# Performance work log

Hardware: AMD Instinct MI355X
Metric: run time of the kernel (lower is better)

The kernel has to match this reference:

```python
import jax, jax.numpy as jnp
import numpy as np

DIM = 768
NUM_HEADS = 12
DIM_HEAD = 64
INNER = NUM_HEADS * DIM_HEAD  # 768
SCALE = DIM_HEAD ** -0.5


def setup_inputs() -> dict:
    key = jax.random.key(0)
    k1, k2, k3 = jax.random.split(key, 3)
    B, N = 8, 1024
    x = jax.random.normal(k1, (B, N, DIM), dtype=jnp.float32)
    # Linear(dim, 3*inner_dim, bias=False): weight shape (out, in) torch-style
    w_qkv = jax.random.normal(k2, (3 * INNER, DIM), dtype=jnp.float32) * (DIM ** -0.5)
    # proj: Linear(inner_dim, dim, bias=False)
    w_proj = jax.random.normal(k3, (DIM, INNER), dtype=jnp.float32) * (INNER ** -0.5)
    return {"x": x, "w_qkv": w_qkv, "w_proj": w_proj}


def reference(x, w_qkv, w_proj):
    B, N, C = x.shape
    H, dh = NUM_HEADS, DIM_HEAD
    # qkv projection: (B,N,C) @ (C, 3*inner) -> (B,N,3*inner)
    qkv = jnp.einsum('bnc,oc->bno', x, w_qkv)
    qkv = qkv.reshape(B, N, 3, H, dh).transpose(2, 0, 3, 1, 4)  # (3,B,H,N,dh)
    q, k, v = qkv[0], qkv[1], qkv[2]
    # attention scores (B,H,N,N)
    attn_scores = jnp.einsum('bhnd,bhmd->bhnm', q, k) * SCALE
    attn_probs = jax.nn.softmax(attn_scores, axis=-1)
    # attention output (B,H,N,dh) -> (B,N,inner)
    attn_out = jnp.einsum('bhnm,bhmd->bhnd', attn_probs, v)
    attn_out = attn_out.transpose(0, 2, 1, 3).reshape(B, N, H * dh)
    out = jnp.einsum('bni,oi->bno', attn_out, w_proj)
    return out
```

## Files before the change

kernel.cpp:

```cpp
#include <hip/hip_runtime.h>
#include <stdint.h>

typedef unsigned short u16;
typedef __attribute__((ext_vector_type(8))) short short8;
typedef __attribute__((ext_vector_type(4))) short short4v;
typedef __attribute__((ext_vector_type(4))) float f32x4;

#define LOG2E 1.44269504088896340736f

#define Bb 8
#define NSEQ 1024
#define DIMC 768
#define NH 12
#define DH 64
#define INNER 768
#define MTOT (Bb*NSEQ)
#define QKVN (3*INNER)
#define HEADS_TOT (Bb*NH)
#define QKV_PART ((size_t)Bb*NH*NSEQ*DH)

static __device__ inline u16 f2bf(float f) {
    uint32_t u = __builtin_bit_cast(uint32_t, f);
    uint32_t r = (u + 0x7fffu + ((u >> 16) & 1u)) >> 16;
    return (u16)r;
}

static __device__ __forceinline__ uint32_t pkbf(float f0, float f1) {
    uint32_t u0 = __builtin_bit_cast(uint32_t, f0) + 0x8000u;
    uint32_t u1 = __builtin_bit_cast(uint32_t, f1) + 0x8000u;
    return __builtin_amdgcn_perm(u1, u0, 0x07060302u);
}

#if __has_builtin(__builtin_amdgcn_mfma_f32_16x16x16bf16_1k)
static __device__ __forceinline__ f32x4 mfma16(short4v a, short4v b, f32x4 c) {
    return __builtin_amdgcn_mfma_f32_16x16x16bf16_1k(a, b, c, 0, 0, 0);
}
#else
static __device__ __forceinline__ f32x4 mfma16(short4v a, short4v b, f32x4 c) {
    asm volatile("v_mfma_f32_16x16x16_bf16 %0, %1, %2, %0\n\ts_nop 7\n\ts_nop 7"
                 : "+v"(c) : "v"(a), "v"(b));
    return c;
}
#endif

typedef __attribute__((address_space(1))) const void gas_void;
typedef __attribute__((address_space(3))) void las_void;
static __device__ __forceinline__ void async16(u16* lds, const u16* g) {
    __builtin_amdgcn_global_load_lds((gas_void*)(uintptr_t)g,
                                     (las_void*)(uintptr_t)lds, 16, 0, 0);
}

template <int N>
static __device__ __forceinline__ void wait_vm() {
    __builtin_amdgcn_s_waitcnt(0x0f70 | N);
}

#define NX8  786432
#define NWQ8 221184
#define NWP8 73728
#define NCVT (NX8 + NWQ8 + NWP8)
__global__ __launch_bounds__(256) void cvt_all(const float* __restrict__ x,
                                               const float* __restrict__ wq,
                                               const float* __restrict__ wp,
                                               u16* __restrict__ xb,
                                               u16* __restrict__ wqb,
                                               u16* __restrict__ wpb) {
    int i = blockIdx.x * 256 + threadIdx.x;
    const float* s; u16* d; int j;
    if (i < NX8) { s = x; d = xb; j = i; }
    else if (i < NX8 + NWQ8) { s = wq; d = wqb; j = i - NX8; }
    else { s = wp; d = wpb; j = i - NX8 - NWQ8; }
    const float4* s4 = (const float4*)s;
    float4 a = s4[2 * j], b = s4[2 * j + 1];
    float v[8] = {a.x, a.y, a.z, a.w, b.x, b.y, b.z, b.w};
    u16 o[8];
#pragma unroll
    for (int t = 0; t < 8; t++) o[t] = f2bf(v[t]);
    ((uint4*)d)[j] = *(const uint4*)o;
}

#define BK 32
__global__ __launch_bounds__(512, 4) void gemm_qkv(const u16* __restrict__ A,
                                                   const u16* __restrict__ Bm,
                                                   u16* __restrict__ qkv) {
    __shared__ u16 As[3][128 * BK];
    __shared__ u16 Bs[3][256 * BK];
    const int tid = threadIdx.x;
    const int w = tid >> 6, lane = tid & 63, quad = lane >> 4, l16 = lane & 15;
    const int wr = w >> 2, wc = w & 3;
    const int bid = blockIdx.x + 9 * blockIdx.y;
    const int xcd = bid & 7, j9 = bid >> 3;
    const int m0 = (8 * xcd + j9 / 9) * 128;
    const int n0 = (j9 % 9) * 256;
    const int K = DIMC;

    const int rl = lane >> 2, cc = lane & 3;
    const int ra = w * 16 + rl;
    const u16* agp = A + (size_t)(m0 + ra) * K + ((cc - ((ra >> 1) & 3)) & 3) * 8;
    const int aslot = (w * 16) * BK;
    const u16* bgp[2]; int bslot[2];
#pragma unroll
    for (int j = 0; j < 2; j++) {
        int rb = w * 32 + j * 16 + rl;
        bgp[j] = Bm + (size_t)(n0 + rb) * K + ((cc - ((rb >> 1) & 3)) & 3) * 8;
        bslot[j] = (w * 32 + j * 16) * BK;
    }

    const int swz = ((quad + ((l16 >> 1) & 3)) & 3) * 8;
    int aoff[4], boff[4];
#pragma unroll
    for (int t = 0; t < 4; t++) {
        aoff[t] = (wr * 64 + t * 16 + l16) * BK + swz;
        boff[t] = (wc * 64 + t * 16 + l16) * BK + swz;
    }

#pragma unroll
    for (int tt = 0; tt < 2; tt++) {
        int kt = tt * BK;
        async16(&As[tt][aslot], agp + kt);
        async16(&Bs[tt][bslot[0]], bgp[0] + kt);
        async16(&Bs[tt][bslot[1]], bgp[1] + kt);
    }

    f32x4 acc[4][4] = {};
    const int NIT = K / BK;
    int cur = 0;
    for (int it = 0; it < NIT; ++it) {
        if (it < NIT - 1) wait_vm<3>();
        else              wait_vm<0>();
        __builtin_amdgcn_s_barrier();
        if (it < NIT - 2) {
            int pre = cur + 2; if (pre >= 3) pre -= 3;
            int ktn = (it + 2) * BK;
            async16(&As[pre][aslot], agp + ktn);
            async16(&Bs[pre][bslot[0]], bgp[0] + ktn);
            async16(&Bs[pre][bslot[1]], bgp[1] + ktn);
        }
        short8 af[4], bf[4];
#pragma unroll
        for (int t = 0; t < 4; t++) af[t] = *(const short8*)(&As[cur][aoff[t]]);
#pragma unroll
        for (int t = 0; t < 4; t++) bf[t] = *(const short8*)(&Bs[cur][boff[t]]);
#pragma unroll
        for (int mt = 0; mt < 4; mt++)
#pragma unroll
            for (int nt = 0; nt < 4; nt++)
                acc[mt][nt] = __builtin_amdgcn_mfma_f32_16x16x32_bf16(af[mt], bf[nt],
                                                                      acc[mt][nt], 0, 0, 0);
        cur = (cur == 2) ? 0 : cur + 1;
    }

#pragma unroll
    for (int nt = 0; nt < 4; nt++) {
        int o = n0 + wc * 64 + nt * 16 + l16;
        int which = o / 768;
        int rem = o - which * 768;
        int h = rem >> 6, d = rem & 63;
        if (which == 2) {
            u16* vt = qkv + 2 * QKV_PART;
#pragma unroll
            for (int mt = 0; mt < 4; mt++) {
                int m = m0 + wr * 64 + mt * 16 + quad * 4;
                int bb = m >> 10, ns = m & 1023;
                alignas(8) u16 pk[4];
#pragma unroll
                for (int r = 0; r < 4; r++) pk[r] = f2bf(acc[mt][nt][r]);
                *(uint2*)(vt + ((size_t)(bb * NH + h) * DH + d) * NSEQ + ns) =
                    *(const uint2*)pk;
            }
        } else {
            float sc = (which == 0) ? (0.125f * LOG2E) : 1.0f;
#pragma unroll
            for (int mt = 0; mt < 4; mt++)
#pragma unroll
                for (int r = 0; r < 4; r++) {
                    int m = m0 + wr * 64 + mt * 16 + quad * 4 + r;
                    int bb = m >> 10, ns = m & 1023;
                    size_t idx = (size_t)which * QKV_PART +
                                 (((size_t)(bb * NH + h) * NSEQ + ns) << 6) + d;
                    qkv[idx] = f2bf(acc[mt][nt][r] * sc);
                }
        }
    }
}

#define PBM 64
#define PBN 128
__global__ __launch_bounds__(256) void gemm_proj(const u16* __restrict__ A,
                                                 const u16* __restrict__ Bm,
                                                 float* __restrict__ Co) {
    __shared__ u16 As[3][PBM * BK];
    __shared__ u16 Bs[3][PBN * BK];
    const int tid = threadIdx.x;
    const int w = tid >> 6, lane = tid & 63, quad = lane >> 4, l16 = lane & 15;
    const int wr = w >> 1, wc = w & 1;
    const int m0 = blockIdx.y * PBM;
    const int n0 = blockIdx.x * PBN;
    const int K = INNER, N = DIMC;

    const int rl = lane >> 2, cc = lane & 3;
    const int ra = w * 16 + rl;
    const u16* agp = A + (size_t)(m0 + ra) * K + ((cc - ((ra >> 1) & 3)) & 3) * 8;
    const int aslot = (w * 16) * BK;
    const u16* bgp[2]; int bslot[2];
#pragma unroll
    for (int j = 0; j < 2; j++) {
        int rb = j * 64 + w * 16 + rl;
        bgp[j] = Bm + (size_t)(n0 + rb) * K + ((cc - ((rb >> 1) & 3)) & 3) * 8;
        bslot[j] = (j * 64 + w * 16) * BK;
    }
    const int swz = ((quad + ((l16 >> 1) & 3)) & 3) * 8;
    int aoff[2], boff[4];
#pragma unroll
    for (int t = 0; t < 2; t++) aoff[t] = (wr * 32 + t * 16 + l16) * BK + swz;
#pragma unroll
    for (int t = 0; t < 4; t++) boff[t] = (wc * 64 + t * 16 + l16) * BK + swz;

#pragma unroll
    for (int tt = 0; tt < 2; tt++) {
        int kt = tt * BK;
        async16(&As[tt][aslot], agp + kt);
        async16(&Bs[tt][bslot[0]], bgp[0] + kt);
        async16(&Bs[tt][bslot[1]], bgp[1] + kt);
    }

    f32x4 acc[2][4] = {};
    const int NIT = K / BK;
    int cur = 0;
    for (int it = 0; it < NIT; ++it) {
        if (it < NIT - 1) wait_vm<3>(); else wait_vm<0>();
        __builtin_amdgcn_s_barrier();
        if (it < NIT - 2) {
            int pre = cur + 2; if (pre >= 3) pre -= 3;
            int ktn = (it + 2) * BK;
            async16(&As[pre][aslot], agp + ktn);
            async16(&Bs[pre][bslot[0]], bgp[0] + ktn);
            async16(&Bs[pre][bslot[1]], bgp[1] + ktn);
        }
        short8 af[2], bf[4];
#pragma unroll
        for (int t = 0; t < 2; t++) af[t] = *(const short8*)(&As[cur][aoff[t]]);
#pragma unroll
        for (int t = 0; t < 4; t++) bf[t] = *(const short8*)(&Bs[cur][boff[t]]);
#pragma unroll
        for (int mt = 0; mt < 2; mt++)
#pragma unroll
            for (int nt = 0; nt < 4; nt++)
                acc[mt][nt] = __builtin_amdgcn_mfma_f32_16x16x32_bf16(af[mt], bf[nt],
                                                                      acc[mt][nt], 0, 0, 0);
        cur = (cur == 2) ? 0 : cur + 1;
    }
#pragma unroll
    for (int mt = 0; mt < 2; mt++)
#pragma unroll
        for (int nt = 0; nt < 4; nt++) {
            int o = n0 + wc * 64 + nt * 16 + l16;
#pragma unroll
            for (int r = 0; r < 4; r++) {
                int m = m0 + wr * 32 + mt * 16 + quad * 4 + r;
                Co[(size_t)m * N + o] = acc[mt][nt][r];
            }
        }
}

__global__ __launch_bounds__(256) void attn_kernel(const u16* __restrict__ qkv,
                                                   u16* __restrict__ attn) {
    __shared__ u16 Ks[3][64 * 64];
    __shared__ u16 Vs[3][64 * 64];

    const int tid = threadIdx.x;
    const int w = tid >> 6, lane = tid & 63, quad = lane >> 4, l16 = lane & 15;
    const int bh = blockIdx.x, qt = blockIdx.y;
    const size_t headoff = (size_t)bh * NSEQ * DH;
    const u16* Qp = qkv + headoff;
    const u16* Kp = qkv + QKV_PART + headoff;
    const u16* Vtp = qkv + 2 * QKV_PART + headoff;
    const int q0 = qt * 128 + w * 32;

    const int rl8 = lane >> 3, cc8 = lane & 7;
    const u16* kg[2]; const u16* vg[2]; int ksl[2];
#pragma unroll
    for (int j = 0; j < 2; j++) {
        int r = w * 16 + j * 8 + rl8;
        int c = ((cc8 - r) & 7) * 8;
        kg[j] = Kp + (size_t)r * DH + c;
        vg[j] = Vtp + (size_t)r * NSEQ + c;
        ksl[j] = (w * 16 + j * 8) * 64;
    }

    const int sw0 = ((quad + l16) & 7) * 8;
    const int sw1 = ((quad + 4 + l16) & 7) * 8;

    short8 qf[2][2];
#pragma unroll
    for (int mf = 0; mf < 2; mf++) {
        qf[mf][0] = *(const short8*)(Qp + (size_t)(q0 + mf * 16 + l16) * DH + quad * 8);
        qf[mf][1] = *(const short8*)(Qp + (size_t)(q0 + mf * 16 + l16) * DH + 32 + quad * 8);
    }

#pragma unroll
    for (int tt = 0; tt < 3; tt++) {
        int kt = tt * 64;
#pragma unroll
        for (int j = 0; j < 2; j++) {
            async16(&Ks[tt][ksl[j]], kg[j] + (size_t)kt * DH);
            async16(&Vs[tt][ksl[j]], vg[j] + kt);
        }
    }
    asm volatile("" :: "v"(qf[0][0]), "v"(qf[0][1]), "v"(qf[1][0]), "v"(qf[1][1]));

    f32x4 oacc[2][4] = {};
    float lsum[2] = {0.f, 0.f};

    const int NIT = NSEQ / 64;
    int cur = 0;
    for (int it = 0; it < NIT; ++it) {
        if (it == 0)          wait_vm<8>();
        else if (it < NIT - 1) wait_vm<4>();
        else                   wait_vm<0>();
        __builtin_amdgcn_s_barrier();
        if (it >= 1 && it < NIT - 2) {
            int pre = cur + 2; if (pre >= 3) pre -= 3;
            int ktn = (it + 2) * 64;
#pragma unroll
            for (int j = 0; j < 2; j++) {
                async16(&Ks[pre][ksl[j]], kg[j] + (size_t)ktn * DH);
                async16(&Vs[pre][ksl[j]], vg[j] + ktn);
            }
        }

        short8 kf[4][2];
#pragma unroll
        for (int nt = 0; nt < 4; nt++) {
            const u16* kr = &Ks[cur][(nt * 16 + l16) * 64];
            kf[nt][0] = *(const short8*)(kr + sw0);
            kf[nt][1] = *(const short8*)(kr + sw1);
        }
        short4v vf[4][4];
#pragma unroll
        for (int nt2 = 0; nt2 < 4; nt2++) {
            int row = nt2 * 16 + l16;
#pragma unroll
            for (int c = 0; c < 4; c++) {
                int off = row * 64 + (((c * 2 + (quad >> 1) + row) & 7) << 3) + (quad & 1) * 4;
                vf[nt2][c] = *(const short4v*)(&Vs[cur][off]);
            }
        }

#pragma unroll
        for (int mf = 0; mf < 2; mf++) {
            f32x4 st[4];
#pragma unroll
            for (int nt = 0; nt < 4; nt++) {
                f32x4 z = {};
                z = __builtin_amdgcn_mfma_f32_16x16x32_bf16(kf[nt][0], qf[mf][0], z, 0, 0, 0);
                z = __builtin_amdgcn_mfma_f32_16x16x32_bf16(kf[nt][1], qf[mf][1], z, 0, 0, 0);
                st[nt] = z;
            }
            short4v pf[4];
#pragma unroll
            for (int c = 0; c < 4; c++) {
                float p0 = __builtin_amdgcn_exp2f(st[c][0]);
                float p1 = __builtin_amdgcn_exp2f(st[c][1]);
                float p2 = __builtin_amdgcn_exp2f(st[c][2]);
                float p3 = __builtin_amdgcn_exp2f(st[c][3]);
                lsum[mf] += (p0 + p1) + (p2 + p3);
                uint2 u = {pkbf(p0, p1), pkbf(p2, p3)};
                pf[c] = __builtin_bit_cast(short4v, u);
            }
#pragma unroll
            for (int nt2 = 0; nt2 < 4; nt2++)
#pragma unroll
                for (int c = 0; c < 4; c++)
                    oacc[mf][nt2] = mfma16(vf[nt2][c], pf[c], oacc[mf][nt2]);
        }
        cur = (cur == 2) ? 0 : cur + 1;
    }

#pragma unroll
    for (int mf = 0; mf < 2; mf++) {
        float v = lsum[mf];
        v += __shfl_xor(v, 16);
        v += __shfl_xor(v, 32);
        lsum[mf] = 1.0f / v;
    }

    const int b = bh / NH, h = bh - (bh / NH) * NH;
#pragma unroll
    for (int mf = 0; mf < 2; mf++) {
        int q = q0 + mf * 16 + l16;
        float inv = lsum[mf];
#pragma unroll
        for (int nt2 = 0; nt2 < 4; nt2++) {
            uint2 u = {pkbf(oacc[mf][nt2][0] * inv, oacc[mf][nt2][1] * inv),
                       pkbf(oacc[mf][nt2][2] * inv, oacc[mf][nt2][3] * inv)};
            int d = nt2 * 16 + quad * 4;
            *(uint2*)(attn + ((size_t)(b * NSEQ + q)) * INNER + h * DH + d) = u;
        }
    }
}

extern "C" void kernel_launch(void* const* d_in, const int* in_sizes, int n_in,
                              void* d_out, int out_size, void* d_ws, size_t ws_size,
                              hipStream_t stream) {
    const float* x = (const float*)d_in[0];
    const float* w_qkv = (const float*)d_in[1];
    const float* w_proj = (const float*)d_in[2];
    float* out = (float*)d_out;

    u16* xb = (u16*)d_ws;
    u16* wqkvb = xb + 6291456;
    u16* wprojb = wqkvb + 1769472;
    u16* qkvb = wprojb + 589824;
    u16* attnb = qkvb + 18874368;

    cvt_all<<<NCVT / 256, 256, 0, stream>>>(x, w_qkv, w_proj, xb, wqkvb, wprojb);

    dim3 g1(QKVN / 256, MTOT / 128);
    gemm_qkv<<<g1, 512, 0, stream>>>(xb, wqkvb, qkvb);

    dim3 g2(HEADS_TOT, NSEQ / 128);
    attn_kernel<<<g2, 256, 0, stream>>>(qkvb, attnb);

    dim3 g3(INNER / PBN, MTOT / PBM);
    gemm_proj<<<g3, 256, 0, stream>>>(attnb, wprojb, out);
}
```

Measured before the change: 185.9 us.

## Halve wave count per block in all kernels, doubling per-wave tile work

Each of the three main kernels (QKV GEMM, attention, projection GEMM) now runs with half as many waves per block. Each wave computes twice as many output rows (8x4 or 4x4 MFMA tiles, four query fragments in attention), and load issue counts and waitcnt thresholds are adjusted to match. It also adds s_setprio around MFMA bursts and a sched_barrier after the block barrier, and fixes the waitcnt encoding for counts above 15. The aim is more register-level reuse of loaded fragments and fewer barrier participants, at the cost of higher register pressure and fewer waves to hide latency.

```diff
diff --git a/kernel.cpp b/kernel.cpp
--- a/kernel.cpp
+++ b/kernel.cpp
@@ -52,7 +52,13 @@
 
 template <int N>
 static __device__ __forceinline__ void wait_vm() {
-    __builtin_amdgcn_s_waitcnt(0x0f70 | N);
+    constexpr int simm = 0x0f70 | (N & 15) | ((N >> 4) << 14);
+    __builtin_amdgcn_s_waitcnt(simm);
+}
+
+static __device__ __forceinline__ void block_barrier() {
+    __builtin_amdgcn_s_barrier();
+    __builtin_amdgcn_sched_barrier(0);
 }
 
 #define NX8  786432
@@ -80,14 +86,13 @@
 }
 
 #define BK 32
-__global__ __launch_bounds__(512, 4) void gemm_qkv(const u16* __restrict__ A,
+__global__ __launch_bounds__(256, 2) void gemm_qkv(const u16* __restrict__ A,
                                                    const u16* __restrict__ Bm,
                                                    u16* __restrict__ qkv) {
     __shared__ u16 As[3][128 * BK];
     __shared__ u16 Bs[3][256 * BK];
     const int tid = threadIdx.x;
     const int w = tid >> 6, lane = tid & 63, quad = lane >> 4, l16 = lane & 15;
-    const int wr = w >> 2, wc = w & 3;
     const int bid = blockIdx.x + 9 * blockIdx.y;
     const int xcd = bid & 7, j9 = bid >> 3;
     const int m0 = (8 * xcd + j9 / 9) * 128;
@@ -95,72 +100,79 @@
     const int K = DIMC;
 
     const int rl = lane >> 2, cc = lane & 3;
-    const int ra = w * 16 + rl;
-    const u16* agp = A + (size_t)(m0 + ra) * K + ((cc - ((ra >> 1) & 3)) & 3) * 8;
-    const int aslot = (w * 16) * BK;
-    const u16* bgp[2]; int bslot[2];
+    const u16* agp[2]; int aslot[2];
 #pragma unroll
     for (int j = 0; j < 2; j++) {
-        int rb = w * 32 + j * 16 + rl;
-        bgp[j] = Bm + (size_t)(n0 + rb) * K + ((cc - ((rb >> 1) & 3)) & 3) * 8;
-        bslot[j] = (w * 32 + j * 16) * BK;
+        int r = j * 64 + w * 16 + rl;
+        agp[j] = A + (size_t)(m0 + r) * K + ((cc - ((r >> 1) & 3)) & 3) * 8;
+        aslot[j] = (j * 64 + w * 16) * BK;
+    }
+    const u16* bgp[4]; int bslot[4];
+#pragma unroll
+    for (int j = 0; j < 4; j++) {
+        int r = j * 64 + w * 16 + rl;
+        bgp[j] = Bm + (size_t)(n0 + r) * K + ((cc - ((r >> 1) & 3)) & 3) * 8;
+        bslot[j] = (j * 64 + w * 16) * BK;
     }
 
     const int swz = ((quad + ((l16 >> 1) & 3)) & 3) * 8;
-    int aoff[4], boff[4];
-#pragma unroll
-    for (int t = 0; t < 4; t++) {
-        aoff[t] = (wr * 64 + t * 16 + l16) * BK + swz;
-        boff[t] = (wc * 64 + t * 16 + l16) * BK + swz;
-    }
+    int aoff[8], boff[4];
+#pragma unroll
+    for (int t = 0; t < 8; t++) aoff[t] = (t * 16 + l16) * BK + swz;
+#pragma unroll
+    for (int t = 0; t < 4; t++) boff[t] = (w * 64 + t * 16 + l16) * BK + swz;
 
 #pragma unroll
     for (int tt = 0; tt < 2; tt++) {
         int kt = tt * BK;
-        async16(&As[tt][aslot], agp + kt);
-        async16(&Bs[tt][bslot[0]], bgp[0] + kt);
-        async16(&Bs[tt][bslot[1]], bgp[1] + kt);
-    }
-
-    f32x4 acc[4][4] = {};
+#pragma unroll
+        for (int j = 0; j < 2; j++) async16(&As[tt][aslot[j]], agp[j] + kt);
+#pragma unroll
+        for (int j = 0; j < 4; j++) async16(&Bs[tt][bslot[j]], bgp[j] + kt);
+    }
+
+    f32x4 acc[8][4] = {};
     const int NIT = K / BK;
     int cur = 0;
     for (int it = 0; it < NIT; ++it) {
-        if (it < NIT - 1) wait_vm<3>();
+        if (it < NIT - 1) wait_vm<6>();
         else              wait_vm<0>();
-        __builtin_amdgcn_s_barrier();
+        block_barrier();
         if (it < NIT - 2) {
             int pre = cur + 2; if (pre >= 3) pre -= 3;
             int ktn = (it + 2) * BK;
-            async16(&As[pre][aslot], agp + ktn);
-            async16(&Bs[pre][bslot[0]], bgp[0] + ktn);
-            async16(&Bs[pre][bslot[1]], bgp[1] + ktn);
-        }
-        short8 af[4], bf[4];
-#pragma unroll
-        for (int t = 0; t < 4; t++) af[t] = *(const short8*)(&As[cur][aoff[t]]);
+#pragma unroll
+            for (int j = 0; j < 2; j++) async16(&As[pre][aslot[j]], agp[j] + ktn);
+#pragma unroll
+            for (int j = 0; j < 4; j++) async16(&Bs[pre][bslot[j]], bgp[j] + ktn);
+        }
+        short8 bf[4], af[8];
 #pragma unroll
         for (int t = 0; t < 4; t++) bf[t] = *(const short8*)(&Bs[cur][boff[t]]);
 #pragma unroll
-        for (int mt = 0; mt < 4; mt++)
+        for (int t = 0; t < 8; t++) af[t] = *(const short8*)(&As[cur][aoff[t]]);
+        __builtin_amdgcn_s_setprio(1);
+#pragma unroll
+        for (int mt = 0; mt < 8; mt++)
 #pragma unroll
             for (int nt = 0; nt < 4; nt++)
                 acc[mt][nt] = __builtin_amdgcn_mfma_f32_16x16x32_bf16(af[mt], bf[nt],
                                                                       acc[mt][nt], 0, 0, 0);
+        __builtin_amdgcn_s_setprio(0);
         cur = (cur == 2) ? 0 : cur + 1;
     }
 
 #pragma unroll
     for (int nt = 0; nt < 4; nt++) {
-        int o = n0 + wc * 64 + nt * 16 + l16;
+        int o = n0 + w * 64 + nt * 16 + l16;
         int which = o / 768;
         int rem = o - which * 768;
         int h = rem >> 6, d = rem & 63;
         if (which == 2) {
             u16* vt = qkv + 2 * QKV_PART;
 #pragma unroll
-            for (int mt = 0; mt < 4; mt++) {
-                int m = m0 + wr * 64 + mt * 16 + quad * 4;
+            for (int mt = 0; mt < 8; mt++) {
+                int m = m0 + mt * 16 + quad * 4;
                 int bb = m >> 10, ns = m & 1023;
                 alignas(8) u16 pk[4];
 #pragma unroll
@@ -171,10 +183,10 @@
         } else {
             float sc = (which == 0) ? (0.125f * LOG2E) : 1.0f;
 #pragma unroll
-            for (int mt = 0; mt < 4; mt++)
+            for (int mt = 0; mt < 8; mt++)
 #pragma unroll
                 for (int r = 0; r < 4; r++) {
-                    int m = m0 + wr * 64 + mt * 16 + quad * 4 + r;
+                    int m = m0 + mt * 16 + quad * 4 + r;
                     int bb = m >> 10, ns = m & 1023;
                     size_t idx = (size_t)which * QKV_PART +
                                  (((size_t)(bb * NH + h) * NSEQ + ns) << 6) + d;
@@ -186,84 +198,91 @@
 
 #define PBM 64
 #define PBN 128
-__global__ __launch_bounds__(256) void gemm_proj(const u16* __restrict__ A,
+__global__ __launch_bounds__(128) void gemm_proj(const u16* __restrict__ A,
                                                  const u16* __restrict__ Bm,
                                                  float* __restrict__ Co) {
     __shared__ u16 As[3][PBM * BK];
     __shared__ u16 Bs[3][PBN * BK];
     const int tid = threadIdx.x;
     const int w = tid >> 6, lane = tid & 63, quad = lane >> 4, l16 = lane & 15;
-    const int wr = w >> 1, wc = w & 1;
     const int m0 = blockIdx.y * PBM;
     const int n0 = blockIdx.x * PBN;
     const int K = INNER, N = DIMC;
 
     const int rl = lane >> 2, cc = lane & 3;
-    const int ra = w * 16 + rl;
-    const u16* agp = A + (size_t)(m0 + ra) * K + ((cc - ((ra >> 1) & 3)) & 3) * 8;
-    const int aslot = (w * 16) * BK;
-    const u16* bgp[2]; int bslot[2];
+    const u16* agp[2]; int aslot[2];
 #pragma unroll
     for (int j = 0; j < 2; j++) {
-        int rb = j * 64 + w * 16 + rl;
-        bgp[j] = Bm + (size_t)(n0 + rb) * K + ((cc - ((rb >> 1) & 3)) & 3) * 8;
-        bslot[j] = (j * 64 + w * 16) * BK;
+        int r = j * 32 + w * 16 + rl;
+        agp[j] = A + (size_t)(m0 + r) * K + ((cc - ((r >> 1) & 3)) & 3) * 8;
+        aslot[j] = (j * 32 + w * 16) * BK;
+    }
+    const u16* bgp[4]; int bslot[4];
+#pragma unroll
+    for (int j = 0; j < 4; j++) {
+        int r = j * 32 + w * 16 + rl;
+        bgp[j] = Bm + (size_t)(n0 + r) * K + ((cc - ((r >> 1) & 3)) & 3) * 8;
+        bslot[j] = (j * 32 + w * 16) * BK;
     }
     const int swz = ((quad + ((l16 >> 1) & 3)) & 3) * 8;
-    int aoff[2], boff[4];
-#pragma unroll
-    for (int t = 0; t < 2; t++) aoff[t] = (wr * 32 + t * 16 + l16) * BK + swz;
-#pragma unroll
-    for (int t = 0; t < 4; t++) boff[t] = (wc * 64 + t * 16 + l16) * BK + swz;
+    int aoff[4], boff[4];
+#pragma unroll
+    for (int t = 0; t < 4; t++) aoff[t] = (t * 16 + l16) * BK + swz;
+#pragma unroll
+    for (int t = 0; t < 4; t++) boff[t] = (w * 64 + t * 16 + l16) * BK + swz;
 
 #pragma unroll
     for (int tt = 0; tt < 2; tt++) {
         int kt = tt * BK;
-        async16(&As[tt][aslot], agp + kt);
-        async16(&Bs[tt][bslot[0]], bgp[0] + kt);
-        async16(&Bs[tt][bslot[1]], bgp[1] + kt);
-    }
-
-    f32x4 acc[2][4] = {};
+#pragma unroll
+        for (int j = 0; j < 2; j++) async16(&As[tt][aslot[j]], agp[j] + kt);
+#pragma unroll
+        for (int j = 0; j < 4; j++) async16(&Bs[tt][bslot[j]], bgp[j] + kt);
+    }
+
+    f32x4 acc[4][4] = {};
     const int NIT = K / BK;
     int cur = 0;
     for (int it = 0; it < NIT; ++it) {
-        if (it < NIT - 1) wait_vm<3>(); else wait_vm<0>();
-        __builtin_amdgcn_s_barrier();
+        if (it < NIT - 1) wait_vm<6>(); else wait_vm<0>();
+        block_barrier();
         if (it < NIT - 2) {
             int pre = cur + 2; if (pre >= 3) pre -= 3;
             int ktn = (it + 2) * BK;
-            async16(&As[pre][aslot], agp + ktn);
-            async16(&Bs[pre][bslot[0]], bgp[0] + ktn);
-            async16(&Bs[pre][bslot[1]], bgp[1] + ktn);
-        }
-        short8 af[2], bf[4];
-#pragma unroll
-        for (int t = 0; t < 2; t++) af[t] = *(const short8*)(&As[cur][aoff[t]]);
+#pragma unroll
+            for (int j = 0; j < 2; j++) async16(&As[pre][aslot[j]], agp[j] + ktn);
+#pragma unroll
+            for (int j = 0; j < 4; j++) async16(&Bs[pre][bslot[j]], bgp[j] + ktn);
+        }
+        short8 af[4], bf[4];
 #pragma unroll
         for (int t = 0; t < 4; t++) bf[t] = *(const short8*)(&Bs[cur][boff[t]]);
 #pragma unroll
-        for (int mt = 0; mt < 2; mt++)
+        for (int t = 0; t < 4; t++) af[t] = *(const short8*)(&As[cur][aoff[t]]);
+        __builtin_amdgcn_s_setprio(1);
+#pragma unroll
+        for (int mt = 0; mt < 4; mt++)
 #pragma unroll
             for (int nt = 0; nt < 4; nt++)
                 acc[mt][nt] = __builtin_amdgcn_mfma_f32_16x16x32_bf16(af[mt], bf[nt],
                                                                       acc[mt][nt], 0, 0, 0);
+        __builtin_amdgcn_s_setprio(0);
         cur = (cur == 2) ? 0 : cur + 1;
     }
 #pragma unroll
-    for (int mt = 0; mt < 2; mt++)
+    for (int mt = 0; mt < 4; mt++)
 #pragma unroll
         for (int nt = 0; nt < 4; nt++) {
-            int o = n0 + wc * 64 + nt * 16 + l16;
+            int o = n0 + w * 64 + nt * 16 + l16;
 #pragma unroll
             for (int r = 0; r < 4; r++) {
-                int m = m0 + wr * 32 + mt * 16 + quad * 4 + r;
+                int m = m0 + mt * 16 + quad * 4 + r;
                 Co[(size_t)m * N + o] = acc[mt][nt][r];
             }
         }
 }
 
-__global__ __launch_bounds__(256) void attn_kernel(const u16* __restrict__ qkv,
+__global__ __launch_bounds__(128) void attn_kernel(const u16* __restrict__ qkv,
                                                    u16* __restrict__ attn) {
     __shared__ u16 Ks[3][64 * 64];
     __shared__ u16 Vs[3][64 * 64];
@@ -275,55 +294,56 @@
     const u16* Qp = qkv + headoff;
     const u16* Kp = qkv + QKV_PART + headoff;
     const u16* Vtp = qkv + 2 * QKV_PART + headoff;
-    const int q0 = qt * 128 + w * 32;
+    const int q0 = qt * 128 + w * 64;
 
     const int rl8 = lane >> 3, cc8 = lane & 7;
-    const u16* kg[2]; const u16* vg[2]; int ksl[2];
-#pragma unroll
-    for (int j = 0; j < 2; j++) {
-        int r = w * 16 + j * 8 + rl8;
+    const u16* kg[4]; const u16* vg[4]; int ksl[4];
+#pragma unroll
+    for (int j = 0; j < 4; j++) {
+        int r = w * 32 + j * 8 + rl8;
         int c = ((cc8 - r) & 7) * 8;
         kg[j] = Kp + (size_t)r * DH + c;
         vg[j] = Vtp + (size_t)r * NSEQ + c;
-        ksl[j] = (w * 16 + j * 8) * 64;
+        ksl[j] = (w * 32 + j * 8) * 64;
     }
 
     const int sw0 = ((quad + l16) & 7) * 8;
     const int sw1 = ((quad + 4 + l16) & 7) * 8;
 
-    short8 qf[2][2];
-#pragma unroll
-    for (int mf = 0; mf < 2; mf++) {
+    short8 qf[4][2];
+#pragma unroll
+    for (int mf = 0; mf < 4; mf++) {
         qf[mf][0] = *(const short8*)(Qp + (size_t)(q0 + mf * 16 + l16) * DH + quad * 8);
         qf[mf][1] = *(const short8*)(Qp + (size_t)(q0 + mf * 16 + l16) * DH + 32 + quad * 8);
     }
+    asm volatile("" :: "v"(qf[0][0]), "v"(qf[0][1]), "v"(qf[1][0]), "v"(qf[1][1]),
+                       "v"(qf[2][0]), "v"(qf[2][1]), "v"(qf[3][0]), "v"(qf[3][1]));
 
 #pragma unroll
     for (int tt = 0; tt < 3; tt++) {
         int kt = tt * 64;
 #pragma unroll
-        for (int j = 0; j < 2; j++) {
+        for (int j = 0; j < 4; j++) {
             async16(&Ks[tt][ksl[j]], kg[j] + (size_t)kt * DH);
             async16(&Vs[tt][ksl[j]], vg[j] + kt);
         }
     }
-    asm volatile("" :: "v"(qf[0][0]), "v"(qf[0][1]), "v"(qf[1][0]), "v"(qf[1][1]));
-
-    f32x4 oacc[2][4] = {};
-    float lsum[2] = {0.f, 0.f};
+
+    f32x4 oacc[4][4] = {};
+    float lsum[4] = {0.f, 0.f, 0.f, 0.f};
 
     const int NIT = NSEQ / 64;
     int cur = 0;
     for (int it = 0; it < NIT; ++it) {
-        if (it == 0)          wait_vm<8>();
-        else if (it < NIT - 1) wait_vm<4>();
+        if (it == 0)           wait_vm<16>();
+        else if (it < NIT - 1) wait_vm<8>();
         else                   wait_vm<0>();
-        __builtin_amdgcn_s_barrier();
+        block_barrier();
         if (it >= 1 && it < NIT - 2) {
             int pre = cur + 2; if (pre >= 3) pre -= 3;
             int ktn = (it + 2) * 64;
 #pragma unroll
-            for (int j = 0; j < 2; j++) {
+            for (int j = 0; j < 4; j++) {
                 async16(&Ks[pre][ksl[j]], kg[j] + (size_t)ktn * DH);
                 async16(&Vs[pre][ksl[j]], vg[j] + ktn);
             }
@@ -348,8 +368,9 @@
         }
 
 #pragma unroll
-        for (int mf = 0; mf < 2; mf++) {
+        for (int mf = 0; mf < 4; mf++) {
             f32x4 st[4];
+            __builtin_amdgcn_s_setprio(1);
 #pragma unroll
             for (int nt = 0; nt < 4; nt++) {
                 f32x4 z = {};
@@ -357,6 +378,7 @@
                 z = __builtin_amdgcn_mfma_f32_16x16x32_bf16(kf[nt][1], qf[mf][1], z, 0, 0, 0);
                 st[nt] = z;
             }
+            __builtin_amdgcn_s_setprio(0);
             short4v pf[4];
 #pragma unroll
             for (int c = 0; c < 4; c++) {
@@ -368,17 +390,19 @@
                 uint2 u = {pkbf(p0, p1), pkbf(p2, p3)};
                 pf[c] = __builtin_bit_cast(short4v, u);
             }
+            __builtin_amdgcn_s_setprio(1);
 #pragma unroll
             for (int nt2 = 0; nt2 < 4; nt2++)
 #pragma unroll
                 for (int c = 0; c < 4; c++)
                     oacc[mf][nt2] = mfma16(vf[nt2][c], pf[c], oacc[mf][nt2]);
+            __builtin_amdgcn_s_setprio(0);
         }
         cur = (cur == 2) ? 0 : cur + 1;
     }
 
 #pragma unroll
-    for (int mf = 0; mf < 2; mf++) {
+    for (int mf = 0; mf < 4; mf++) {
         float v = lsum[mf];
         v += __shfl_xor(v, 16);
         v += __shfl_xor(v, 32);
@@ -387,7 +411,7 @@
 
     const int b = bh / NH, h = bh - (bh / NH) * NH;
 #pragma unroll
-    for (int mf = 0; mf < 2; mf++) {
+    for (int mf = 0; mf < 4; mf++) {
         int q = q0 + mf * 16 + l16;
         float inv = lsum[mf];
 #pragma unroll
@@ -417,11 +441,11 @@
     cvt_all<<<NCVT / 256, 256, 0, stream>>>(x, w_qkv, w_proj, xb, wqkvb, wprojb);
 
     dim3 g1(QKVN / 256, MTOT / 128);
-    gemm_qkv<<<g1, 512, 0, stream>>>(xb, wqkvb, qkvb);
+    gemm_qkv<<<g1, 256, 0, stream>>>(xb, wqkvb, qkvb);
 
     dim3 g2(HEADS_TOT, NSEQ / 128);
-    attn_kernel<<<g2, 256, 0, stream>>>(qkvb, attnb);
+    attn_kernel<<<g2, 128, 0, stream>>>(qkvb, attnb);
 
     dim3 g3(INNER / PBN, MTOT / PBM);
-    gemm_proj<<<g3, 256, 0, stream>>>(attnb, wprojb, out);
-}
+    gemm_proj<<<g3, 128, 0, stream>>>(attnb, wprojb, out);
+}
```

Measured after the change: 193.7 us. +4.2%, slower.

## Software-pipeline QKV GEMM with 4-stage buffers and register double-buffered fragments

Applied to the files above, without the earlier changes.

Moves the QKV projection GEMM to a 4-deep LDS ring with a 2x unrolled loop. Fragments for the next k-tile are read from LDS into a second register set while the MFMAs for the current tile run, and the MFMA block is raised in priority with s_setprio. Barriers gain a sched_barrier so the compiler cannot move memory ops across them, and the attention kernel issues its Q loads before the async K/V prefetch and simplifies its first wait count. The extra LDS and registers halve the occupancy hint on the GEMM, and wait_vm now encodes counts above 15.

```diff
diff --git a/kernel.cpp b/kernel.cpp
--- a/kernel.cpp
+++ b/kernel.cpp
@@ -52,7 +52,13 @@
 
 template <int N>
 static __device__ __forceinline__ void wait_vm() {
-    __builtin_amdgcn_s_waitcnt(0x0f70 | N);
+    constexpr int simm = 0x0f70 | (N & 15) | ((N >> 4) << 14);
+    __builtin_amdgcn_s_waitcnt(simm);
+}
+
+static __device__ __forceinline__ void block_barrier() {
+    __builtin_amdgcn_s_barrier();
+    __builtin_amdgcn_sched_barrier(0);
 }
 
 #define NX8  786432
@@ -80,11 +86,11 @@
 }
 
 #define BK 32
-__global__ __launch_bounds__(512, 4) void gemm_qkv(const u16* __restrict__ A,
+__global__ __launch_bounds__(512, 2) void gemm_qkv(const u16* __restrict__ A,
                                                    const u16* __restrict__ Bm,
                                                    u16* __restrict__ qkv) {
-    __shared__ u16 As[3][128 * BK];
-    __shared__ u16 Bs[3][256 * BK];
+    __shared__ u16 As[4][128 * BK];
+    __shared__ u16 Bs[4][256 * BK];
     const int tid = threadIdx.x;
     const int w = tid >> 6, lane = tid & 63, quad = lane >> 4, l16 = lane & 15;
     const int wr = w >> 2, wc = w & 3;
@@ -114,40 +120,52 @@
         boff[t] = (wc * 64 + t * 16 + l16) * BK + swz;
     }
 
-#pragma unroll
-    for (int tt = 0; tt < 2; tt++) {
-        int kt = tt * BK;
-        async16(&As[tt][aslot], agp + kt);
-        async16(&Bs[tt][bslot[0]], bgp[0] + kt);
-        async16(&Bs[tt][bslot[1]], bgp[1] + kt);
-    }
-
     f32x4 acc[4][4] = {};
     const int NIT = K / BK;
-    int cur = 0;
-    for (int it = 0; it < NIT; ++it) {
-        if (it < NIT - 1) wait_vm<3>();
-        else              wait_vm<0>();
-        __builtin_amdgcn_s_barrier();
-        if (it < NIT - 2) {
-            int pre = cur + 2; if (pre >= 3) pre -= 3;
-            int ktn = (it + 2) * BK;
-            async16(&As[pre][aslot], agp + ktn);
-            async16(&Bs[pre][bslot[0]], bgp[0] + ktn);
-            async16(&Bs[pre][bslot[1]], bgp[1] + ktn);
-        }
-        short8 af[4], bf[4];
-#pragma unroll
-        for (int t = 0; t < 4; t++) af[t] = *(const short8*)(&As[cur][aoff[t]]);
-#pragma unroll
-        for (int t = 0; t < 4; t++) bf[t] = *(const short8*)(&Bs[cur][boff[t]]);
+
+    auto issue = [&](int t) {
+        int b = t & 3;
+        int kt = t * BK;
+        async16(&As[b][aslot], agp + kt);
+        async16(&Bs[b][bslot[0]], bgp[0] + kt);
+        async16(&Bs[b][bslot[1]], bgp[1] + kt);
+    };
+    auto rdfrag = [&](int t, short8* af, short8* bf) {
+        const u16* Abase = As[t & 3];
+        const u16* Bbase = Bs[t & 3];
+#pragma unroll
+        for (int i = 0; i < 4; i++) af[i] = *(const short8*)(Abase + aoff[i]);
+#pragma unroll
+        for (int i = 0; i < 4; i++) bf[i] = *(const short8*)(Bbase + boff[i]);
+    };
+    auto mfma_step = [&](short8* af, short8* bf) {
+        __builtin_amdgcn_s_setprio(1);
 #pragma unroll
         for (int mt = 0; mt < 4; mt++)
 #pragma unroll
             for (int nt = 0; nt < 4; nt++)
                 acc[mt][nt] = __builtin_amdgcn_mfma_f32_16x16x32_bf16(af[mt], bf[nt],
                                                                       acc[mt][nt], 0, 0, 0);
-        cur = (cur == 2) ? 0 : cur + 1;
+        __builtin_amdgcn_s_setprio(0);
+    };
+
+    issue(0); issue(1); issue(2);
+    wait_vm<6>();
+    block_barrier();
+    short8 af0[4], bf0[4], af1[4], bf1[4];
+    rdfrag(0, af0, bf0);
+
+    for (int it = 0; it < NIT; it += 2) {
+        if (it < NIT - 2) wait_vm<3>(); else wait_vm<0>();
+        block_barrier();
+        if (it + 3 < NIT) issue(it + 3);
+        if (it + 1 < NIT) rdfrag(it + 1, af1, bf1);
+        mfma_step(af0, bf0);
+        if (it + 1 < NIT - 2) wait_vm<3>(); else wait_vm<0>();
+        block_barrier();
+        if (it + 4 < NIT) issue(it + 4);
+        if (it + 2 < NIT) rdfrag(it + 2, af0, bf0);
+        mfma_step(af1, bf1);
     }
 
 #pragma unroll
@@ -229,7 +247,7 @@
     int cur = 0;
     for (int it = 0; it < NIT; ++it) {
         if (it < NIT - 1) wait_vm<3>(); else wait_vm<0>();
-        __builtin_amdgcn_s_barrier();
+        block_barrier();
         if (it < NIT - 2) {
             int pre = cur + 2; if (pre >= 3) pre -= 3;
             int ktn = (it + 2) * BK;
@@ -297,6 +315,7 @@
         qf[mf][0] = *(const short8*)(Qp + (size_t)(q0 + mf * 16 + l16) * DH + quad * 8);
         qf[mf][1] = *(const short8*)(Qp + (size_t)(q0 + mf * 16 + l16) * DH + 32 + quad * 8);
     }
+    asm volatile("" :: "v"(qf[0][0]), "v"(qf[0][1]), "v"(qf[1][0]), "v"(qf[1][1]));
 
 #pragma unroll
     for (int tt = 0; tt < 3; tt++) {
@@ -307,7 +326,6 @@
             async16(&Vs[tt][ksl[j]], vg[j] + kt);
         }
     }
-    asm volatile("" :: "v"(qf[0][0]), "v"(qf[0][1]), "v"(qf[1][0]), "v"(qf[1][1]));
 
     f32x4 oacc[2][4] = {};
     float lsum[2] = {0.f, 0.f};
@@ -315,10 +333,9 @@
     const int NIT = NSEQ / 64;
     int cur = 0;
     for (int it = 0; it < NIT; ++it) {
-        if (it == 0)          wait_vm<8>();
-        else if (it < NIT - 1) wait_vm<4>();
-        else                   wait_vm<0>();
-        __builtin_amdgcn_s_barrier();
+        if (it < NIT - 1) wait_vm<4>();
+        else              wait_vm<0>();
+        block_barrier();
         if (it >= 1 && it < NIT - 2) {
             int pre = cur + 2; if (pre >= 3) pre -= 3;
             int ktn = (it + 2) * 64;
```

After: 186.3 us. No clear change (+0.2%).
